# Optimization experiments

Measured on AMD Instinct MI355X. Metric: run time of the kernel, lower is better.

The kernel has to match this reference:

```python
import jax, jax.numpy as jnp
from jax import lax
import numpy as np

VOCAB, EMB, HID, NOUT = 32000, 256, 512, 5
SEQ, BATCH = 512, 64


def setup_inputs() -> dict:
    key = jax.random.key(0)
    ks = jax.random.split(key, 9)
    s = 1.0 / np.sqrt(HID)
    seq = jax.random.randint(ks[0], (SEQ, BATCH), 0, VOCAB, dtype=jnp.int32)
    # pack_padded_sequence expects descending lengths; values in [1, SEQ]
    lengths = jnp.sort(jax.random.randint(ks[1], (BATCH,), 1, SEQ + 1, dtype=jnp.int32))[::-1]
    return {
        "seq": seq,
        "lengths": lengths,
        "emb": jax.random.normal(ks[2], (VOCAB, EMB), jnp.float32),
        "w_ih": jax.random.uniform(ks[3], (3 * HID, EMB), jnp.float32, -s, s),
        "w_hh": jax.random.uniform(ks[4], (3 * HID, HID), jnp.float32, -s, s),
        "b_ih": jax.random.uniform(ks[5], (3 * HID,), jnp.float32, -s, s),
        "b_hh": jax.random.uniform(ks[6], (3 * HID,), jnp.float32, -s, s),
        "w_out": jax.random.uniform(ks[7], (NOUT, HID), jnp.float32, -s, s),
        "b_out": jax.random.uniform(ks[8], (NOUT,), jnp.float32, -s, s),
    }


def reference(seq, lengths, emb, w_ih, w_hh, b_ih, b_hh, w_out, b_out):
    S, B = seq.shape
    H = w_hh.shape[1]
    x = emb[seq]                                            # (S, B, E)
    # precompute all input-side gate projections in one GEMM
    x_gates = jnp.einsum('sbe,ge->sbg', x, w_ih) + b_ih     # (S, B, 3H)

    def step(h, inp):
        xg, t = inp                                         # xg: (B, 3H)
        hg = h @ w_hh.T + b_hh                              # (B, 3H)
        xr, xz, xn = jnp.split(xg, 3, axis=-1)
        hr, hz, hn = jnp.split(hg, 3, axis=-1)
        r = jax.nn.sigmoid(xr + hr)
        z = jax.nn.sigmoid(xz + hz)
        n = jnp.tanh(xn + r * hn)
        h_new = (1.0 - z) * n + z * h
        # packed sequence semantics: freeze hidden past each sequence's length
        valid = (t < lengths)[:, None]
        h_out = jnp.where(valid, h_new, h)
        return h_out, None

    h0 = jnp.zeros((B, H), x.dtype)
    h_last, _ = lax.scan(step, h0, (x_gates, jnp.arange(S)))
    logits = h_last @ w_out.T + b_out                       # (B, NOUT)
    return jax.nn.log_softmax(logits, axis=-1)
```

## Files before the change

### kernel.cpp

```cpp
#include <hip/hip_runtime.h>


typedef unsigned short ushort_t;
typedef short short8      __attribute__((ext_vector_type(8)));
typedef float floatx4     __attribute__((ext_vector_type(4)));
typedef unsigned int uintx4 __attribute__((ext_vector_type(4)));
typedef unsigned short ushort4v __attribute__((ext_vector_type(4)));
typedef _Float16 half8    __attribute__((ext_vector_type(8)));

#define SEQL 512
#define BATCH 64
#define EMBD 256
#define HID 512
#define G3 1536
#define NOUT 5
#define NGRP 8
#define GRPB 8
#define GSLOT 8192
#define TSLOT 65536
#define RING2 131072
#define XG_BYTES 100663296
#define PROGN 512
#define FLAGN 256
#define ZERON (PROGN + FLAGN)
#define BAD_LIMIT 8

__device__ __forceinline__ float bf2f(ushort_t v){
  union { unsigned u; float f; } x; x.u = ((unsigned)v) << 16; return x.f;
}
__device__ __forceinline__ ushort_t f2bf(float f){
  unsigned u = __float_as_uint(f);
  return (ushort_t)((u + 0x7FFFu + ((u >> 16) & 1u)) >> 16);
}
__device__ __forceinline__ float sigm(float x){
  x = fminf(fmaxf(x, -20.f), 20.f);
  return 1.f / (1.f + __expf(-x));
}
__device__ __forceinline__ float tanh_c(float x){
  x = fminf(fmaxf(x, -10.f), 10.f);
  float e = __expf(2.f * x);
  return (e - 1.f) / (e + 1.f);
}
__device__ __forceinline__ bool has_sent(half8 v){
  union { half8 h; unsigned u[4]; } x; x.h = v;
  bool b = false;
  #pragma unroll
  for (int i = 0; i < 4; ++i){
    b |= ((x.u[i] & 0xFFFFu) == 0xFFFFu);
    b |= ((x.u[i] >> 16) == 0xFFFFu);
  }
  return b;
}

__global__ __launch_bounds__(256) void gru_init(char* __restrict__ rings,
                                                int* __restrict__ prog){
  size_t i = ((size_t)blockIdx.x * 256 + threadIdx.x) * 16;
  uintx4 s = {0xFFFFFFFFu, 0xFFFFFFFFu, 0xFFFFFFFFu, 0xFFFFFFFFu};
  const char* p = rings + i;
  asm volatile("global_store_dwordx4 %0, %1, off sc0 sc1" :: "v"(p), "v"(s) : "memory");
  if (blockIdx.x == 0){
    int z = 0;
    for (int k = threadIdx.x; k < ZERON; k += 256){
      asm volatile("global_store_dword %0, %1, off sc0 sc1"
                   :: "v"(prog + k), "v"(z) : "memory");
    }
  }
}

#define LDSIDX2(row, chunk) (((row) << 7) + ((((chunk) ^ ((row) & 7))) << 3))
__global__ __launch_bounds__(256) void gru_xgates(
    const int* __restrict__ seq, const float* __restrict__ emb,
    const float* __restrict__ w_ih, const float* __restrict__ b_ih,
    ushort_t* __restrict__ xg)
{
  __shared__ __align__(16) short lA[64 * 128];
  __shared__ __align__(16) short lB[64 * 128];
  const int tid   = threadIdx.x;
  const int sIdx  = blockIdx.x;
  const int nBase = blockIdx.y * 64;
  const int w    = tid >> 6;
  const int l    = tid & 63;
  const int l15  = l & 15;
  const int quad = l >> 4;
  floatx4 acc[4] = {};

  #pragma unroll
  for (int kp = 0; kp < 2; ++kp){
    __syncthreads();
    #pragma unroll
    for (int i = 0; i < 4; ++i){
      int lin = i * 256 + tid;
      int row = lin >> 4;
      int kc  = lin & 15;
      int kbase = kp * 128 + kc * 8;
      int token = seq[(sIdx << 6) + row];
      const float* srcA = emb  + (size_t)token * EMBD + kbase;
      const float* srcB = w_ih + (size_t)(nBase + row) * EMBD + kbase;
      floatx4 a0 = *(const floatx4*)(srcA);
      floatx4 a1 = *(const floatx4*)(srcA + 4);
      floatx4 b0 = *(const floatx4*)(srcB);
      floatx4 b1 = *(const floatx4*)(srcB + 4);
      short8 pa, pb;
      #pragma unroll
      for (int j = 0; j < 4; ++j){
        pa[j]     = (short)f2bf(a0[j]);
        pa[j + 4] = (short)f2bf(a1[j]);
        pb[j]     = (short)f2bf(b0[j]);
        pb[j + 4] = (short)f2bf(b1[j]);
      }
      *(short8*)&lA[LDSIDX2(row, kc)] = pa;
      *(short8*)&lB[LDSIDX2(row, kc)] = pb;
    }
    __syncthreads();
    #pragma unroll
    for (int kc = 0; kc < 4; ++kc){
      int chunk = kc * 4 + quad;
      short8 a = *(const short8*)&lA[LDSIDX2(w * 16 + l15, chunk)];
      #pragma unroll
      for (int s = 0; s < 4; ++s){
        short8 bf = *(const short8*)&lB[LDSIDX2(s * 16 + l15, chunk)];
        acc[s] = __builtin_amdgcn_mfma_f32_16x16x32_bf16(a, bf, acc[s], 0, 0, 0);
      }
    }
  }
  #pragma unroll
  for (int s = 0; s < 4; ++s){
    int g = nBase + s * 16 + l15;
    float bias = b_ih[g];
    ushort4v pk;
    #pragma unroll
    for (int r = 0; r < 4; ++r) pk[r] = f2bf(acc[s][r] + bias);
    *(ushort4v*)(xg + ((size_t)sIdx * G3 + g) * BATCH + (w * 16 + quad * 4)) = pk;
  }
}

__global__ __launch_bounds__(256, 1) void gru_rec(
    const ushort_t* __restrict__ xg, const float* __restrict__ whh,
    const float* __restrict__ bhh, const int* __restrict__ lengths,
    char* __restrict__ truth, char* __restrict__ fastr,
    int* __restrict__ prog, int depth)
{
  __shared__ __align__(16) _Float16 wlds[48 * 64 * 8];
  __shared__ __align__(16) _Float16 hscr[4 * 256];
  __shared__ int s_grp, s_slc, s_fast;
  const int tid  = threadIdx.x;
  const int w    = tid >> 6;
  const int l    = tid & 63;
  const int l15  = l & 15;
  const int quad = l >> 4;
  int* flags = prog + PROGN;

  int* regs = prog + 384;
  if (tid == 0){
    unsigned xcd;
    asm volatile("s_getreg_b32 %0, hwreg(HW_REG_XCC_ID)" : "=s"(xcd));
    xcd &= 7u;
    int myx = atomicAdd(&regs[1 + xcd], 1);
    asm volatile("s_waitcnt vmcnt(0)" ::: "memory");
    int gt = atomicAdd(&regs[0], 1);
    int v;
    do {
      asm volatile("s_sleep 1" ::: "memory");
      asm volatile("global_load_dword %0, %1, off sc0 sc1\n\t"
                   "s_waitcnt vmcnt(0)"
                   : "=v"(v) : "v"(&regs[0]) : "memory");
    } while (v < 256);
    int ok = 1;
    #pragma unroll
    for (int x = 0; x < 8; ++x){
      int c;
      asm volatile("global_load_dword %0, %1, off sc0 sc1\n\t"
                   "s_waitcnt vmcnt(0)"
                   : "=v"(c) : "v"(&regs[1 + x]) : "memory");
      ok &= (c == 32);
    }
    s_fast = ok;
    s_grp  = ok ? (int)xcd : 0;
    s_slc  = ok ? (myx & 31) : gt;
  }
  __syncthreads();
  const int fast = s_fast;
  const int grp  = s_grp;
  const int g0   = s_slc;
  if (!fast && g0 >= 32) return;
  const int g = g0 & 31;
  const int j = g * 16 + l15;

  #pragma unroll
  for (int i = 0; i < 12; ++i){
    int p  = i * 4 + w;
    int G  = p >> 4;
    int ks = p & 15;
    const float* src = whh + (size_t)(G * HID + j) * HID + ks * 32 + quad * 8;
    floatx4 f0 = *(const floatx4*)(src);
    floatx4 f1 = *(const floatx4*)(src + 4);
    half8 hv;
    #pragma unroll
    for (int q = 0; q < 4; ++q){ hv[q] = (_Float16)f0[q]; hv[q + 4] = (_Float16)f1[q]; }
    *(half8*)&wlds[((size_t)p * 64 + l) * 8] = hv;
  }
  __syncthreads();
  if (fast && tid >= 64) return;

  char* fastb = fastr + (size_t)grp * depth * GSLOT;
  const int locb = fast ? ((quad & 1) * 4) : (quad * 4);
  const int gb   = fast ? (grp * GRPB + locb) : (w * 16 + locb);
  const int arow = l15 & 7;
  const int trow = fast ? (grp * GRPB + (l15 & 7)) : (w * 16 + l15);
  const float bhR = bhh[j], bhZ = bhh[HID + j], bhN = bhh[2 * HID + j];
  int   len[4];
  float h[4];
  #pragma unroll
  for (int r = 0; r < 4; ++r){ len[r] = lengths[gb + r]; h[r] = 0.f; }
  const int Lmax  = lengths[0];
  const int mask  = depth - 1;
  const bool reuse = (depth < Lmax);
  const int flagmode = fast && !reuse;
  const int* fpoll = flags + grp * 32 + (l & 31);
  int* fpub = flags + grp * 32 + g;
  int cmin = 0;
  int badcnt = 0;
  int fastpoll = flagmode;

  for (int t = 0; t < Lmax; ++t){
    if (reuse && t >= depth){
      int target = t - depth + 2;
      if (cmin < target){
        int tgt2 = target + 4;
        if (fast){
          const int* pp = prog + 128 + grp * 32 + (l & 31);
          while (true){
            int p0;
            asm volatile("global_load_dword %0, %1, off sc0 sc1\n\t"
                         "s_waitcnt vmcnt(0)"
                         : "=v"(p0) : "v"(pp) : "memory");
            if (__all(p0 >= tgt2)) break;
            __builtin_amdgcn_s_sleep(2);
          }
        } else {
          while (true){
            int p0, p1;
            asm volatile("global_load_dword %0, %2, off sc0 sc1\n\t"
                         "global_load_dword %1, %3, off sc0 sc1\n\t"
                         "s_waitcnt vmcnt(0)"
                         : "=v"(p0), "=v"(p1) : "v"(prog + l), "v"(prog + 64 + l)
                         : "memory");
            if (__all(p0 >= tgt2 && p1 >= tgt2)) break;
            __builtin_amdgcn_s_sleep(2);
          }
        }
        cmin = tgt2;
      }
    }

    const ushort_t* xt = xg + (size_t)t * G3 * BATCH;
    ushort4v xR = __builtin_nontemporal_load(
        (const ushort4v*)(xt + (size_t)(          j) * BATCH + gb));
    ushort4v xZ = __builtin_nontemporal_load(
        (const ushort4v*)(xt + (size_t)(HID     + j) * BATCH + gb));
    ushort4v xN = __builtin_nontemporal_load(
        (const ushort4v*)(xt + (size_t)(2 * HID + j) * BATCH + gb));

    floatx4 aR = {0.f,0.f,0.f,0.f}, aZ = {0.f,0.f,0.f,0.f}, aN = {0.f,0.f,0.f,0.f};
    if (t > 0){
      const int slotp = (t - 1) & mask;
      const char* rowf = fastb + (size_t)slotp * GSLOT
                       + (size_t)arow * 1024 + quad * 16;
      const char* rowt = truth + (size_t)slotp * TSLOT
                       + (size_t)trow * 1024 + quad * 16;
      half8 aF[16];
      bool good = false;
      if (fastpoll){
        int miss = 0;
        while (true){
          int fv;
          asm volatile("global_load_dword %0, %1, off sc0 sc1\n\t"
                       "s_waitcnt vmcnt(0)"
                       : "=v"(fv) : "v"(fpoll) : "memory");
          if (__all(fv >= t)) break;
          ++miss;
          if (miss > 64) __builtin_amdgcn_s_sleep(8);
          else           __builtin_amdgcn_s_sleep(1);
        }
        #pragma unroll
        for (int ks = 0; ks < 16; ++ks){
          const char* pa = rowf + ks * 64;
          asm volatile("global_load_dwordx4 %0, %1, off sc0"
                       : "=v"(aF[ks]) : "v"(pa) : "memory");
        }
        asm volatile("s_waitcnt vmcnt(0)"
                     : "+v"(aF[0]),  "+v"(aF[1]),  "+v"(aF[2]),  "+v"(aF[3]),
                       "+v"(aF[4]),  "+v"(aF[5]),  "+v"(aF[6]),  "+v"(aF[7]),
                       "+v"(aF[8]),  "+v"(aF[9]),  "+v"(aF[10]), "+v"(aF[11]),
                       "+v"(aF[12]), "+v"(aF[13]), "+v"(aF[14]), "+v"(aF[15])
                     :: "memory");
        bool bad = false;
        #pragma unroll
        for (int ks = 0; ks < 16; ++ks) bad |= has_sent(aF[ks]);
        good = !__any(bad);
        if (!good && ++badcnt >= BAD_LIMIT) fastpoll = 0;
      }
      if (!good){
        int rounds = 0;
        while (true){
          if (rounds){
            if (rounds > 64) __builtin_amdgcn_s_sleep(8);
            else             __builtin_amdgcn_s_sleep(2);
          }
          ++rounds;
          #pragma unroll
          for (int ks = 0; ks < 16; ++ks){
            const char* pa = rowt + ks * 64;
            asm volatile("global_load_dwordx4 %0, %1, off sc0 sc1"
                         : "=v"(aF[ks]) : "v"(pa) : "memory");
          }
          asm volatile("s_waitcnt vmcnt(0)"
                       : "+v"(aF[0]),  "+v"(aF[1]),  "+v"(aF[2]),  "+v"(aF[3]),
                         "+v"(aF[4]),  "+v"(aF[5]),  "+v"(aF[6]),  "+v"(aF[7]),
                         "+v"(aF[8]),  "+v"(aF[9]),  "+v"(aF[10]), "+v"(aF[11]),
                         "+v"(aF[12]), "+v"(aF[13]), "+v"(aF[14]), "+v"(aF[15])
                       :: "memory");
          bool bad = false;
          #pragma unroll
          for (int ks = 0; ks < 16; ++ks) bad |= has_sent(aF[ks]);
          if (!__any(bad)) break;
        }
      }
      #pragma unroll
      for (int ks = 0; ks < 16; ++ks){
        half8 a  = aF[ks];
        half8 b0 = *(const half8*)&wlds[((size_t)(0 * 16 + ks) * 64 + l) * 8];
        half8 b1 = *(const half8*)&wlds[((size_t)(1 * 16 + ks) * 64 + l) * 8];
        half8 b2 = *(const half8*)&wlds[((size_t)(2 * 16 + ks) * 64 + l) * 8];
        aR = __builtin_amdgcn_mfma_f32_16x16x32_f16(a, b0, aR, 0, 0, 0);
        aZ = __builtin_amdgcn_mfma_f32_16x16x32_f16(a, b1, aZ, 0, 0, 0);
        aN = __builtin_amdgcn_mfma_f32_16x16x32_f16(a, b2, aN, 0, 0, 0);
      }
      if (reuse){
        uintx4 sv = {0xFFFFFFFFu, 0xFFFFFFFFu, 0xFFFFFFFFu, 0xFFFFFFFFu};
        if (!fast || l15 < 8){
          #pragma unroll
          for (int ks = 0; ks < 16; ++ks){
            const char* pt = rowt + ks * 64;
            asm volatile("global_store_dwordx4 %0, %1, off sc0 sc1"
                         :: "v"(pt), "v"(sv) : "memory");
          }
        }
      }
    }

    #pragma unroll
    for (int r = 0; r < 4; ++r){
      float rr = sigm(bf2f(xR[r]) + aR[r] + bhR);
      float zz = sigm(bf2f(xZ[r]) + aZ[r] + bhZ);
      float nn = tanh_c(bf2f(xN[r]) + rr * (aN[r] + bhN));
      float hn = (1.f - zz) * nn + zz * h[r];
      h[r] = (t < len[r]) ? hn : h[r];
    }

    _Float16* scr = hscr + w * 256;
    if (!fast || quad < 2){
      #pragma unroll
      for (int r = 0; r < 4; ++r) scr[(locb + r) * 16 + l15] = (_Float16)h[r];
    }
    asm volatile("s_waitcnt lgkmcnt(0)" ::: "memory");
    if (flagmode){
      if (l < 16){
        int bl = l >> 1;
        int hc = l & 1;
        half8 ch = *(const half8*)&scr[bl * 16 + hc * 8];
        const char* df = fastb + (size_t)(t & mask) * GSLOT
                       + (size_t)bl * 1024 + (size_t)g * 32 + (size_t)hc * 16;
        asm volatile("global_store_dwordx4 %0, %1, off sc0"
                     :: "v"(df), "v"(ch) : "memory");
      }
      asm volatile("s_waitcnt vmcnt(0)" ::: "memory");
      if (l == 0){
        int pv = t + 1;
        asm volatile("global_store_dword %0, %1, off sc0 sc1"
                     :: "v"(fpub), "v"(pv) : "memory");
      }
      if (l < 16){
        int bl = l >> 1;
        int hc = l & 1;
        half8 ch = *(const half8*)&scr[bl * 16 + hc * 8];
        const char* dt = truth + (size_t)(t & mask) * TSLOT
                       + (size_t)(grp * GRPB + bl) * 1024
                       + (size_t)g * 32 + (size_t)hc * 16;
        asm volatile("global_store_dwordx4 %0, %1, off sc0 sc1"
                     :: "v"(dt), "v"(ch) : "memory");
      }
    } else {
      const int pubN = fast ? 16 : 32;
      if (l < pubN){
        int bl = l >> 1;
        int hc = l & 1;
        half8 ch = *(const half8*)&scr[bl * 16 + hc * 8];
        int gbatch = fast ? (grp * GRPB + bl) : (w * 16 + bl);
        const char* dt = truth + (size_t)(t & mask) * TSLOT
                       + (size_t)gbatch * 1024 + (size_t)g * 32 + (size_t)hc * 16;
        asm volatile("global_store_dwordx4 %0, %1, off sc0 sc1"
                     :: "v"(dt), "v"(ch) : "memory");
      }
      if (reuse && ((t & 7) == 7)){
        asm volatile("s_waitcnt vmcnt(0)" ::: "memory");
        if (l == 0){
          int pv = t + 1;
          const int* pp = fast ? (prog + 128 + grp * 32 + g) : (prog + w * 32 + g);
          asm volatile("global_store_dword %0, %1, off sc0 sc1"
                       :: "v"(pp), "v"(pv) : "memory");
        }
      }
    }
  }
}

__global__ __launch_bounds__(64) void gru_out(
    const char* __restrict__ truth, const int* __restrict__ lengths,
    const float* __restrict__ wout, const float* __restrict__ bout,
    float* __restrict__ out, int depth)
{
  const int b = blockIdx.x, l = threadIdx.x;
  const int Lmax = lengths[0];
  const _Float16* h = (const _Float16*)(truth
      + (size_t)((Lmax - 1) & (depth - 1)) * TSLOT + (size_t)b * 1024);
  half8 hv = *(const half8*)(h + l * 8);
  float p[NOUT];
  #pragma unroll
  for (int o = 0; o < NOUT; ++o){
    const float* wr = wout + o * HID + l * 8;
    float a = 0.f;
    #pragma unroll
    for (int i = 0; i < 8; ++i) a += wr[i] * (float)hv[i];
    #pragma unroll
    for (int d = 32; d >= 1; d >>= 1) a += __shfl_down(a, d, 64);
    p[o] = a;
  }
  if (l == 0){
    float lg[NOUT], m = -1e30f;
    #pragma unroll
    for (int o = 0; o < NOUT; ++o){
      float v = p[o] + bout[o];
      if (!(v == v)) v = -1.0f;
      lg[o] = v; m = fmaxf(m, v);
    }
    float ssum = 0.f;
    #pragma unroll
    for (int o = 0; o < NOUT; ++o) ssum += __expf(lg[o] - m);
    float ls = __logf(ssum);
    #pragma unroll
    for (int o = 0; o < NOUT; ++o) out[b * NOUT + o] = lg[o] - m - ls;
  }
}

extern "C" void kernel_launch(void* const* d_in, const int* in_sizes, int n_in,
                              void* d_out, int out_size, void* d_ws, size_t ws_size,
                              hipStream_t stream) {
  (void)in_sizes; (void)n_in; (void)out_size;
  const int*   seq     = (const int*)d_in[0];
  const int*   lengths = (const int*)d_in[1];
  const float* emb     = (const float*)d_in[2];
  const float* w_ih    = (const float*)d_in[3];
  const float* w_hh    = (const float*)d_in[4];
  const float* b_ih    = (const float*)d_in[5];
  const float* b_hh    = (const float*)d_in[6];
  const float* w_out   = (const float*)d_in[7];
  const float* b_out   = (const float*)d_in[8];
  float*       outp    = (float*)d_out;

  size_t avail = (ws_size > (size_t)XG_BYTES + 32768)
               ? ws_size - (size_t)XG_BYTES - 32768 : 0;
  int depth = 16;
  while (depth < 512 && ((size_t)(depth << 1) * RING2) <= avail) depth <<= 1;

  char* ws = (char*)d_ws;
  ushort_t* xg    = (ushort_t*)ws;
  char*     truth = ws + XG_BYTES;
  char*     fastr = truth + (size_t)depth * TSLOT;
  int*      prog  = (int*)(fastr + (size_t)depth * TSLOT);

  gru_init<<<depth * 32, 256, 0, stream>>>(truth, prog);
  dim3 g1(SEQL, G3 / 64);
  gru_xgates<<<g1, 256, 0, stream>>>(seq, emb, w_ih, b_ih, xg);
  gru_rec<<<256, 256, 0, stream>>>(xg, w_hh, b_hh, lengths, truth, fastr, prog, depth);
  gru_out<<<BATCH, 64, 0, stream>>>(truth, lengths, w_out, b_out, outp, depth);
}
```

Measured before the change: 2.149 ms.

## Add local-scope flag polling path with fallback to system-scope flags

Adds a second set of progress flags that workgroups in a group publish and poll without system-coherence cache bits. Polling uses an agent-scope acquire fence and no sleeps, and falls back to the old sc0/sc1 flag polling after a fixed poll budget. Fast-path hidden-state stores also drop the sc0 bit. This aims to cut the per-step cross-workgroup synchronisation latency in the recurrent loop, at the cost of relying on weaker coherence (cross-XCD visibility risk) and busy spinning.

```diff
diff --git a/kernel.cpp b/kernel.cpp
--- a/kernel.cpp
+++ b/kernel.cpp
@@ -22,8 +22,10 @@
 #define XG_BYTES 100663296
 #define PROGN 512
 #define FLAGN 256
-#define ZERON (PROGN + FLAGN)
+#define FLAG2N 512
+#define ZERON (PROGN + FLAGN + FLAG2N)
 #define BAD_LIMIT 8
+#define POLL_BUDGET 3000
 
 __device__ __forceinline__ float bf2f(ushort_t v){
   union { unsigned u; float f; } x; x.u = ((unsigned)v) << 16; return x.f;
@@ -148,7 +150,8 @@
   const int l    = tid & 63;
   const int l15  = l & 15;
   const int quad = l >> 4;
-  int* flags = prog + PROGN;
+  int* flags_s = prog + PROGN;
+  int* flags_l = prog + PROGN + FLAGN;
 
   int* regs = prog + 384;
   if (tid == 0){
@@ -216,11 +219,13 @@
   const int mask  = depth - 1;
   const bool reuse = (depth < Lmax);
   const int flagmode = fast && !reuse;
-  const int* fpoll = flags + grp * 32 + (l & 31);
-  int* fpub = flags + grp * 32 + g;
+  const int* fpoll_s = flags_s + grp * 32 + (l & 31);
+  int* fpub_s = flags_s + grp * 32 + g;
+  const int* fpoll_l = flags_l + grp * 64 + (l & 31);
+  int* fpub_l = flags_l + grp * 64 + g;
   int cmin = 0;
   int badcnt = 0;
-  int fastpoll = flagmode;
+  int mode = flagmode ? 2 : 0;
 
   for (int t = 0; t < Lmax; ++t){
     if (reuse && t >= depth){
@@ -269,19 +274,33 @@
       const char* rowt = truth + (size_t)slotp * TSLOT
                        + (size_t)trow * 1024 + quad * 16;
       half8 aF[16];
-      bool good = false;
-      if (fastpoll){
+      bool have = false;
+      if (mode == 2){
+        int miss = 0;
+        while (true){
+          __builtin_amdgcn_fence(__ATOMIC_ACQUIRE, "agent");
+          int fv;
+          asm volatile("global_load_dword %0, %1, off\n\t"
+                       "s_waitcnt vmcnt(0)"
+                       : "=v"(fv) : "v"(fpoll_l) : "memory");
+          if (__all(fv >= t)) break;
+          if (++miss > POLL_BUDGET){ mode = 1; break; }
+        }
+      }
+      if (mode == 1){
         int miss = 0;
         while (true){
           int fv;
           asm volatile("global_load_dword %0, %1, off sc0 sc1\n\t"
                        "s_waitcnt vmcnt(0)"
-                       : "=v"(fv) : "v"(fpoll) : "memory");
+                       : "=v"(fv) : "v"(fpoll_s) : "memory");
           if (__all(fv >= t)) break;
           ++miss;
           if (miss > 64) __builtin_amdgcn_s_sleep(8);
           else           __builtin_amdgcn_s_sleep(1);
         }
+      }
+      if (mode >= 1){
         #pragma unroll
         for (int ks = 0; ks < 16; ++ks){
           const char* pa = rowf + ks * 64;
@@ -297,10 +316,10 @@
         bool bad = false;
         #pragma unroll
         for (int ks = 0; ks < 16; ++ks) bad |= has_sent(aF[ks]);
-        good = !__any(bad);
-        if (!good && ++badcnt >= BAD_LIMIT) fastpoll = 0;
-      }
-      if (!good){
+        have = !__any(bad);
+        if (!have && ++badcnt >= BAD_LIMIT) mode = 0;
+      }
+      if (!have){
         int rounds = 0;
         while (true){
           if (rounds){
@@ -371,14 +390,16 @@
         half8 ch = *(const half8*)&scr[bl * 16 + hc * 8];
         const char* df = fastb + (size_t)(t & mask) * GSLOT
                        + (size_t)bl * 1024 + (size_t)g * 32 + (size_t)hc * 16;
-        asm volatile("global_store_dwordx4 %0, %1, off sc0"
+        asm volatile("global_store_dwordx4 %0, %1, off"
                      :: "v"(df), "v"(ch) : "memory");
       }
       asm volatile("s_waitcnt vmcnt(0)" ::: "memory");
       if (l == 0){
         int pv = t + 1;
+        asm volatile("global_store_dword %0, %1, off"
+                     :: "v"(fpub_l), "v"(pv) : "memory");
         asm volatile("global_store_dword %0, %1, off sc0 sc1"
-                     :: "v"(fpub), "v"(pv) : "memory");
+                     :: "v"(fpub_s), "v"(pv) : "memory");
       }
       if (l < 16){
         int bl = l >> 1;
```

Result: slower. 2.767 ms (+28.8%).

## Replace per-step flag handshake with sentinel-polling on fast-path hidden-state buffer

Applied to the files above, without the earlier changes.

The fast path in the persistent GRU recurrence no longer has producers publish a per-group progress flag after storing hidden-state chunks. Consumers instead poll the fast (L2-local, sc0) buffer directly and check for sentinel values, giving up to a bounded local budget before falling back to the coherent truth buffer. This removes a store-wait-flag round trip from the critical path of every timestep. The cost is repeated 16-load sweeps while data is not ready, plus a possible permanent fallback to the slower path after repeated misses.

```diff
diff --git a/kernel.cpp b/kernel.cpp
--- a/kernel.cpp
+++ b/kernel.cpp
@@ -23,7 +23,8 @@
 #define PROGN 512
 #define FLAGN 256
 #define ZERON (PROGN + FLAGN)
-#define BAD_LIMIT 8
+#define LOCAL_BUDGET 64
+#define BADSTEP_LIMIT 6
 
 __device__ __forceinline__ float bf2f(ushort_t v){
   union { unsigned u; float f; } x; x.u = ((unsigned)v) << 16; return x.f;
@@ -148,7 +149,6 @@
   const int l    = tid & 63;
   const int l15  = l & 15;
   const int quad = l >> 4;
-  int* flags = prog + PROGN;
 
   int* regs = prog + 384;
   if (tid == 0){
@@ -215,12 +215,10 @@
   const int Lmax  = lengths[0];
   const int mask  = depth - 1;
   const bool reuse = (depth < Lmax);
-  const int flagmode = fast && !reuse;
-  const int* fpoll = flags + grp * 32 + (l & 31);
-  int* fpub = flags + grp * 32 + g;
+  const int fastpath = fast && !reuse;
+  int localok = fastpath;
+  int badsteps = 0;
   int cmin = 0;
-  int badcnt = 0;
-  int fastpoll = flagmode;
 
   for (int t = 0; t < Lmax; ++t){
     if (reuse && t >= depth){
@@ -269,38 +267,32 @@
       const char* rowt = truth + (size_t)slotp * TSLOT
                        + (size_t)trow * 1024 + quad * 16;
       half8 aF[16];
-      bool good = false;
-      if (fastpoll){
-        int miss = 0;
+      bool got = false;
+      if (localok){
+        int rounds = 0;
         while (true){
-          int fv;
-          asm volatile("global_load_dword %0, %1, off sc0 sc1\n\t"
-                       "s_waitcnt vmcnt(0)"
-                       : "=v"(fv) : "v"(fpoll) : "memory");
-          if (__all(fv >= t)) break;
-          ++miss;
-          if (miss > 64) __builtin_amdgcn_s_sleep(8);
-          else           __builtin_amdgcn_s_sleep(1);
+          #pragma unroll
+          for (int ks = 0; ks < 16; ++ks){
+            const char* pa = rowf + ks * 64;
+            asm volatile("global_load_dwordx4 %0, %1, off sc0"
+                         : "=v"(aF[ks]) : "v"(pa) : "memory");
+          }
+          asm volatile("s_waitcnt vmcnt(0)"
+                       : "+v"(aF[0]),  "+v"(aF[1]),  "+v"(aF[2]),  "+v"(aF[3]),
+                         "+v"(aF[4]),  "+v"(aF[5]),  "+v"(aF[6]),  "+v"(aF[7]),
+                         "+v"(aF[8]),  "+v"(aF[9]),  "+v"(aF[10]), "+v"(aF[11]),
+                         "+v"(aF[12]), "+v"(aF[13]), "+v"(aF[14]), "+v"(aF[15])
+                       :: "memory");
+          bool bad = false;
+          #pragma unroll
+          for (int ks = 0; ks < 16; ++ks) bad |= has_sent(aF[ks]);
+          if (!__any(bad)){ got = true; break; }
+          if (++rounds >= LOCAL_BUDGET) break;
+          if (rounds > 8) __builtin_amdgcn_s_sleep(1);
         }
-        #pragma unroll
-        for (int ks = 0; ks < 16; ++ks){
-          const char* pa = rowf + ks * 64;
-          asm volatile("global_load_dwordx4 %0, %1, off sc0"
-                       : "=v"(aF[ks]) : "v"(pa) : "memory");
-        }
-        asm volatile("s_waitcnt vmcnt(0)"
-                     : "+v"(aF[0]),  "+v"(aF[1]),  "+v"(aF[2]),  "+v"(aF[3]),
-                       "+v"(aF[4]),  "+v"(aF[5]),  "+v"(aF[6]),  "+v"(aF[7]),
-                       "+v"(aF[8]),  "+v"(aF[9]),  "+v"(aF[10]), "+v"(aF[11]),
-                       "+v"(aF[12]), "+v"(aF[13]), "+v"(aF[14]), "+v"(aF[15])
-                     :: "memory");
-        bool bad = false;
-        #pragma unroll
-        for (int ks = 0; ks < 16; ++ks) bad |= has_sent(aF[ks]);
-        good = !__any(bad);
-        if (!good && ++badcnt >= BAD_LIMIT) fastpoll = 0;
-      }
-      if (!good){
+        if (!got && ++badsteps >= BADSTEP_LIMIT) localok = 0;
+      }
+      if (!got){
         int rounds = 0;
         while (true){
           if (rounds){
@@ -364,7 +356,7 @@
       for (int r = 0; r < 4; ++r) scr[(locb + r) * 16 + l15] = (_Float16)h[r];
     }
     asm volatile("s_waitcnt lgkmcnt(0)" ::: "memory");
-    if (flagmode){
+    if (fastpath){
       if (l < 16){
         int bl = l >> 1;
         int hc = l & 1;
@@ -373,17 +365,6 @@
                        + (size_t)bl * 1024 + (size_t)g * 32 + (size_t)hc * 16;
         asm volatile("global_store_dwordx4 %0, %1, off sc0"
                      :: "v"(df), "v"(ch) : "memory");
-      }
-      asm volatile("s_waitcnt vmcnt(0)" ::: "memory");
-      if (l == 0){
-        int pv = t + 1;
-        asm volatile("global_store_dword %0, %1, off sc0 sc1"
-                     :: "v"(fpub), "v"(pv) : "memory");
-      }
-      if (l < 16){
-        int bl = l >> 1;
-        int hc = l & 1;
-        half8 ch = *(const half8*)&scr[bl * 16 + hc * 8];
         const char* dt = truth + (size_t)(t & mask) * TSLOT
                        + (size_t)(grp * GRPB + bl) * 1024
                        + (size_t)g * 32 + (size_t)hc * 16;
```

New measurement: 3.187 ms. 48.3% more time.
